# Optimization experiments

Hardware: AMD Instinct MI355X
Metric: run time of the kernel (lower is better)

The kernel has to match this reference:

```python
import jax, jax.numpy as jnp
import numpy as np

S, B, D = 2048, 2, 1024
NH, DH, DI = 16, 64, 4096


def setup_inputs() -> dict:
    key = jax.random.key(0)
    ks = jax.random.split(key, 12)
    init_qkv = 1.0 / np.sqrt(D)
    init_out = 1.0 / np.sqrt(NH * DH)
    stdm = 1.0 / np.sqrt(D)
    stdi = 1.0 / np.sqrt(DI)

    def u(k, shape, lo, hi):
        return jax.random.uniform(k, shape, jnp.float32, lo, hi)

    inp = {}
    inp["dec_inp"] = jax.random.normal(ks[0], (S, B, D), jnp.float32)
    # causal mask: True = masked (future key j > query i); shape [q, k, batch]
    causal = jnp.triu(jnp.ones((S, S), bool), k=1)
    inp["attn_mask"] = jnp.broadcast_to(causal[:, :, None], (S, S, B))
    inp["query_mean"] = u(ks[1], (NH * DH, D), -init_qkv, init_qkv)
    inp["key_mean"] = u(ks[2], (NH * DH, D), -init_qkv, init_qkv)
    inp["value_mean"] = u(ks[3], (NH * DH, D), -init_qkv, init_qkv)
    inp["query_std"] = u(ks[4], (NH * DH, D), 2 * np.log(init_qkv), np.log(init_qkv))
    inp["key_std"] = u(ks[5], (NH * DH, D), 2 * np.log(init_qkv), np.log(init_qkv))
    inp["value_std"] = u(ks[6], (NH * DH, D), 2 * np.log(init_qkv), np.log(init_qkv))
    inp["output_mean"] = u(ks[7], (D, NH * DH), -init_out, init_out)
    inp["output_std"] = u(ks[8], (D, NH * DH), 2 * np.log(init_out), np.log(init_out))
    inp["ln1_gamma"] = jnp.ones((D,), jnp.float32)
    inp["ln1_beta"] = jnp.zeros((D,), jnp.float32)
    inp["w1_mean"] = u(ks[9], (DI, D), -stdm, stdm)
    inp["w2_mean"] = u(ks[10], (D, DI), -stdi, stdi)
    inp["w1_std"] = u(ks[11], (DI, D), 2 * np.log(stdm), np.log(stdm))
    inp["w2_std"] = u(jax.random.fold_in(key, 99), (D, DI), 2 * np.log(stdi), np.log(stdi))
    inp["ln2_gamma"] = jnp.ones((D,), jnp.float32)
    inp["ln2_beta"] = jnp.zeros((D,), jnp.float32)
    return inp


def _layer_norm(x, g, b, eps=1e-5):
    mu = jnp.mean(x, -1, keepdims=True)
    var = jnp.mean((x - mu) ** 2, -1, keepdims=True)
    return g * (x - mu) * jax.lax.rsqrt(var + eps) + b


def _kl(theta_mean, theta_std):
    return jnp.mean(theta_mean ** 2 - 2.0 * theta_std + jnp.exp(2.0 * theta_std)) / 2.0


def reference(dec_inp, attn_mask, query_mean, key_mean, value_mean, query_std,
              key_std, value_std, output_mean, output_std, ln1_gamma, ln1_beta,
              w1_mean, w2_mean, w1_std, w2_std, ln2_gamma, ln2_beta):
    scale = 1.0 / (DH ** 0.5)
    # QKV projections (eval mode: no Bayesian weight sampling, diffs are 0)
    head_q = jnp.einsum('ibd,hd->ibh', dec_inp, query_mean).reshape(S, B, NH, DH)
    head_k = jnp.einsum('ibd,hd->ibh', dec_inp, key_mean).reshape(S, B, NH, DH)
    head_v = jnp.einsum('ibd,hd->ibh', dec_inp, value_mean).reshape(S, B, NH, DH)
    attn_score = jnp.einsum('ibnd,jbnd->ijbn', head_q, head_k) * scale
    attn_score = jnp.where(attn_mask[:, :, :, None], -jnp.inf, attn_score)
    attn_prob = jax.nn.softmax(attn_score, axis=1)  # softmax over key dim j
    attn_vec = jnp.einsum('ijbn,jbnd->ibnd', attn_prob, head_v).reshape(S, B, NH * DH)
    # NOTE: the original code (bug-faithfully) projects with value_mean, not output_mean
    attn_out = jnp.einsum('ibh,dh->ibd', attn_vec, value_mean)
    h = _layer_norm(dec_inp + attn_out, ln1_gamma, ln1_beta)
    attn_kl = _kl(
        jnp.concatenate([query_mean, key_mean, value_mean, output_mean.T], -1),
        jnp.concatenate([query_std, key_std, value_std, output_std.T], -1))
    # Bayesian positionwise FF (no activation in BayesPositionwiseFF)
    l1 = jnp.einsum('ibd,fd->ibf', h, w1_mean)
    l2 = jnp.einsum('ibf,df->ibd', l1, w2_mean)
    out = _layer_norm(h + l2, ln2_gamma, ln2_beta)
    ff_kl = _kl(jnp.concatenate([w1_mean, w2_mean.T], -1),
                jnp.concatenate([w1_std, w2_std.T], -1))
    return out, attn_kl + ff_kl
```

## Files before the change

kernel.cpp:

```cpp
#include <hip/hip_runtime.h>

#define S_LEN  2048
#define BATCH  2
#define DMODEL 1024
#define NHEADS 16
#define DHEAD  64
#define DFF    4096
#define MROWS  (S_LEN*BATCH)
#define QKVN   3072

typedef __attribute__((ext_vector_type(8))) short bf16x8;
typedef __attribute__((ext_vector_type(4))) float f32x4;
typedef __attribute__((ext_vector_type(4))) short s16x4;

#define NEG_BIG (-3.0e38f)
#define SCALE_LOG2 (0.125f * 1.4426950408889634f)

__device__ __forceinline__ short f2bf(float f){
  unsigned u = __float_as_uint(f);
  u += 0x7fffu + ((u >> 16) & 1u);
  return (short)(u >> 16);
}

__device__ __forceinline__ void gload16(const void* gptr, void* lptr){
  __builtin_amdgcn_global_load_lds(
      (const __attribute__((address_space(1))) unsigned int*)gptr,
      (__attribute__((address_space(3))) unsigned int*)lptr,
      16, 0, 0);
}

__global__ __launch_bounds__(256) void cast_kernel(const float* __restrict__ in,
                                                   short* __restrict__ out, int n){
  int i = (blockIdx.x * 256 + threadIdx.x) * 4;
  if (i >= n) return;
  f32x4 v = *(const f32x4*)(in + i);
  s16x4 o;
  o[0] = f2bf(v[0]); o[1] = f2bf(v[1]); o[2] = f2bf(v[2]); o[3] = f2bf(v[3]);
  *(s16x4*)(out + i) = o;
}

__global__ __launch_bounds__(512) void gemm_bt(const short* __restrict__ A,
                                               const short* __restrict__ Bt,
                                               float* __restrict__ Cf,
                                               short* __restrict__ Cb,
                                               int M, int N, int K){
  __shared__ short As[128][32];
  __shared__ short Bs[128][32];
  const int t = threadIdx.x;
  const int lane = t & 63, w = t >> 6;
  const int m0 = blockIdx.y * 128, n0 = blockIdx.x * 128;
  const int wm = (w & 3) * 32, wn = (w >> 2) * 64;
  const int lr = lane & 15, lg = lane >> 4;

  f32x4 acc[2][4] = {};

  const short* Ap = A  + (size_t)(m0 + (t >> 2)) * K + (t & 3) * 8;
  const short* Bp = Bt + (size_t)(n0 + (t >> 2)) * K + (t & 3) * 8;
  char* ldsA = (char*)(&As[0][0]) + w * 1024;
  char* ldsB = (char*)(&Bs[0][0]) + w * 1024;

  for (int k0 = 0; k0 < K; k0 += 32){
    gload16(Ap + k0, ldsA);
    gload16(Bp + k0, ldsB);
    __syncthreads();
    bf16x8 a0 = *(const bf16x8*)&As[wm      + lr][lg * 8];
    bf16x8 a1 = *(const bf16x8*)&As[wm + 16 + lr][lg * 8];
    bf16x8 b0 = *(const bf16x8*)&Bs[wn      + lr][lg * 8];
    bf16x8 b1 = *(const bf16x8*)&Bs[wn + 16 + lr][lg * 8];
    bf16x8 b2 = *(const bf16x8*)&Bs[wn + 32 + lr][lg * 8];
    bf16x8 b3 = *(const bf16x8*)&Bs[wn + 48 + lr][lg * 8];
    acc[0][0] = __builtin_amdgcn_mfma_f32_16x16x32_bf16(a0, b0, acc[0][0], 0, 0, 0);
    acc[0][1] = __builtin_amdgcn_mfma_f32_16x16x32_bf16(a0, b1, acc[0][1], 0, 0, 0);
    acc[0][2] = __builtin_amdgcn_mfma_f32_16x16x32_bf16(a0, b2, acc[0][2], 0, 0, 0);
    acc[0][3] = __builtin_amdgcn_mfma_f32_16x16x32_bf16(a0, b3, acc[0][3], 0, 0, 0);
    acc[1][0] = __builtin_amdgcn_mfma_f32_16x16x32_bf16(a1, b0, acc[1][0], 0, 0, 0);
    acc[1][1] = __builtin_amdgcn_mfma_f32_16x16x32_bf16(a1, b1, acc[1][1], 0, 0, 0);
    acc[1][2] = __builtin_amdgcn_mfma_f32_16x16x32_bf16(a1, b2, acc[1][2], 0, 0, 0);
    acc[1][3] = __builtin_amdgcn_mfma_f32_16x16x32_bf16(a1, b3, acc[1][3], 0, 0, 0);
    __syncthreads();
  }

  for (int mi = 0; mi < 2; mi++){
    for (int ni = 0; ni < 4; ni++){
      int row = m0 + wm + mi * 16 + lg * 4;
      int col = n0 + wn + ni * 16 + lr;
      for (int r = 0; r < 4; r++){
        float v = acc[mi][ni][r];
        if (Cf) Cf[(size_t)(row + r) * N + col] = v;
        if (Cb) Cb[(size_t)(row + r) * N + col] = f2bf(v);
      }
    }
  }
}

__global__ __launch_bounds__(256) void attn_kernel(const short* __restrict__ QKV,
                                                   short* __restrict__ AV){
  __shared__ short Ks[64][64];
  __shared__ short Vst[64][64];
  __shared__ short Ps[4][16][64];
  const int t = threadIdx.x, lane = t & 63, w = t >> 6;
  const int hb = blockIdx.y;
  const int b = hb >> 4, n = hb & 15;
  const int lr = lane & 15, lg = lane >> 4;

  for (int half = 0; half < 2; half++){
    const int qt = half ? (31 - (int)blockIdx.x) : (int)blockIdx.x;
    const int q0 = qt * 64 + w * 16;

    bf16x8 aq[2];
    {
      const short* qp = QKV + ((size_t)(q0 + lr) * BATCH + b) * QKVN + n * DHEAD + lg * 8;
      aq[0] = *(const bf16x8*)(qp);
      aq[1] = *(const bf16x8*)(qp + 32);
    }

    f32x4 acc[4] = {};
    float m_run[4], l_run[4];
    for (int r = 0; r < 4; r++){ m_run[r] = NEG_BIG; l_run[r] = 0.f; }

    const int njt = qt + 1;
    for (int jt = 0; jt < njt; jt++){
      const int j0 = jt * 64;
      __syncthreads();
      {
        int j = t >> 2, u0 = (t & 3) * 2;
        const short* kp = QKV + ((size_t)(j0 + j) * BATCH + b) * QKVN + DMODEL + n * DHEAD + u0 * 8;
        *(bf16x8*)&Ks[j][(u0 ^ (j & 7)) * 8]       = *(const bf16x8*)(kp);
        *(bf16x8*)&Ks[j][((u0 + 1) ^ (j & 7)) * 8] = *(const bf16x8*)(kp + 8);
        int jv = t & 63, dq = (t >> 6) * 16;
        const short* vp = QKV + ((size_t)(j0 + jv) * BATCH + b) * QKVN + 2 * DMODEL + n * DHEAD + dq;
        bf16x8 v0 = *(const bf16x8*)(vp);
        bf16x8 v1 = *(const bf16x8*)(vp + 8);
        int uj = jv >> 3, jl = jv & 7;
        for (int e = 0; e < 8; e++){
          int sc = (((uj ^ e) << 3) | jl);
          Vst[dq + e][sc]     = v0[e];
          Vst[dq + 8 + e][sc] = v1[e];
        }
      }
      __syncthreads();

      f32x4 s[4];
      __builtin_amdgcn_s_setprio(1);
      for (int nf = 0; nf < 4; nf++){
        f32x4 z = {};
        for (int kk = 0; kk < 2; kk++){
          int row = nf * 16 + lr;
          bf16x8 bk = *(const bf16x8*)&Ks[row][((kk * 4 + lg) ^ (lr & 7)) * 8];
          z = __builtin_amdgcn_mfma_f32_16x16x32_bf16(aq[kk], bk, z, 0, 0, 0);
        }
        s[nf] = z;
      }
      __builtin_amdgcn_s_setprio(0);

      for (int r = 0; r < 4; r++){
        int i_glob = q0 + lg * 4 + r;
        float mx = NEG_BIG;
        for (int nf = 0; nf < 4; nf++){
          int j_glob = j0 + nf * 16 + lr;
          float v = s[nf][r] * SCALE_LOG2;
          if (j_glob > i_glob) v = NEG_BIG;
          s[nf][r] = v;
          mx = fmaxf(mx, v);
        }
        for (int msk = 1; msk < 16; msk <<= 1) mx = fmaxf(mx, __shfl_xor(mx, msk, 64));
        float mn = fmaxf(m_run[r], mx);
        float corr = __builtin_exp2f(m_run[r] - mn);
        m_run[r] = mn;
        l_run[r] *= corr;
        for (int df = 0; df < 4; df++) acc[df][r] *= corr;
      }
      for (int r = 0; r < 4; r++){
        int prow = lg * 4 + r;
        float rs = 0.f;
        for (int nf = 0; nf < 4; nf++){
          float p = __builtin_exp2f(s[nf][r] - m_run[r]);
          rs += p;
          int u = (nf * 2) + (lr >> 3);
          Ps[w][prow][((u ^ (prow & 7)) << 3) | (lr & 7)] = f2bf(p);
        }
        for (int msk = 1; msk < 16; msk <<= 1) rs += __shfl_xor(rs, msk, 64);
        l_run[r] += rs;
      }
      __builtin_amdgcn_s_setprio(1);
      for (int kk = 0; kk < 2; kk++){
        bf16x8 pa = *(const bf16x8*)&Ps[w][lr][((kk * 4 + lg) ^ (lr & 7)) * 8];
        for (int df = 0; df < 4; df++){
          int row = df * 16 + lr;
          bf16x8 bv = *(const bf16x8*)&Vst[row][((kk * 4 + lg) ^ (lr & 7)) * 8];
          acc[df] = __builtin_amdgcn_mfma_f32_16x16x32_bf16(pa, bv, acc[df], 0, 0, 0);
        }
      }
      __builtin_amdgcn_s_setprio(0);
    }

    for (int df = 0; df < 4; df++){
      for (int r = 0; r < 4; r++){
        int i_glob = q0 + lg * 4 + r;
        AV[((size_t)i_glob * BATCH + b) * DMODEL + n * DHEAD + df * 16 + lr] =
            f2bf(acc[df][r] / l_run[r]);
      }
    }
    __syncthreads();
  }
}

__global__ __launch_bounds__(256) void ln_kernel(const float* __restrict__ xa,
                                                 const float* __restrict__ xb,
                                                 const float* __restrict__ gamma,
                                                 const float* __restrict__ beta,
                                                 float* __restrict__ outF,
                                                 short* __restrict__ outB){
  __shared__ float red[4];
  const int row = blockIdx.x, t = threadIdx.x;
  const size_t base = (size_t)row * DMODEL + t * 4;
  f32x4 a  = *(const f32x4*)(xa + base);
  f32x4 bb = *(const f32x4*)(xb + base);
  f32x4 x;
  for (int e = 0; e < 4; e++) x[e] = a[e] + bb[e];
  float sum = x[0] + x[1] + x[2] + x[3];
  for (int m = 1; m < 64; m <<= 1) sum += __shfl_xor(sum, m, 64);
  if ((t & 63) == 0) red[t >> 6] = sum;
  __syncthreads();
  float mu = (red[0] + red[1] + red[2] + red[3]) * (1.f / DMODEL);
  float sq = 0.f;
  for (int e = 0; e < 4; e++){ float d = x[e] - mu; sq += d * d; }
  for (int m = 1; m < 64; m <<= 1) sq += __shfl_xor(sq, m, 64);
  __syncthreads();
  if ((t & 63) == 0) red[t >> 6] = sq;
  __syncthreads();
  float var = (red[0] + red[1] + red[2] + red[3]) * (1.f / DMODEL);
  float rstd = rsqrtf(var + 1e-5f);
  f32x4 g  = *(const f32x4*)(gamma + t * 4);
  f32x4 be = *(const f32x4*)(beta + t * 4);
  for (int e = 0; e < 4; e++){
    float y = g[e] * (x[e] - mu) * rstd + be[e];
    if (outF) outF[base + e] = y;
    if (outB) outB[base + e] = f2bf(y);
  }
}

__global__ __launch_bounds__(256) void kl_kernel(const float* __restrict__ mean,
                                                 const float* __restrict__ stdv,
                                                 int n, double* acc){
  __shared__ double red[4];
  double local = 0.0;
  int stride = gridDim.x * 256;
  for (int i = blockIdx.x * 256 + threadIdx.x; i < n; i += stride){
    float m = mean[i], s = stdv[i];
    local += (double)(m * m) - 2.0 * (double)s + (double)expf(2.f * s);
  }
  for (int msk = 1; msk < 64; msk <<= 1) local += __shfl_xor(local, msk, 64);
  const int t = threadIdx.x;
  if ((t & 63) == 0) red[t >> 6] = local;
  __syncthreads();
  if (t == 0) atomicAdd(acc, red[0] + red[1] + red[2] + red[3]);
}

__global__ void kl_final(const double* acc, float* out){
  out[0] = (float)(acc[0] / 8388608.0 + acc[1] / 16777216.0);
}

extern "C" void kernel_launch(void* const* d_in, const int* in_sizes, int n_in,
                              void* d_out, int out_size, void* d_ws, size_t ws_size,
                              hipStream_t stream){
  (void)in_sizes; (void)n_in; (void)out_size; (void)ws_size;
  const float* dec = (const float*)d_in[0];
  const float* qm  = (const float*)d_in[2];
  const float* km  = (const float*)d_in[3];
  const float* vm  = (const float*)d_in[4];
  const float* qs  = (const float*)d_in[5];
  const float* ks  = (const float*)d_in[6];
  const float* vs  = (const float*)d_in[7];
  const float* om  = (const float*)d_in[8];
  const float* os_ = (const float*)d_in[9];
  const float* g1  = (const float*)d_in[10];
  const float* b1  = (const float*)d_in[11];
  const float* w1m = (const float*)d_in[12];
  const float* w2m = (const float*)d_in[13];
  const float* w1s = (const float*)d_in[14];
  const float* w2s = (const float*)d_in[15];
  const float* g2  = (const float*)d_in[16];
  const float* b2  = (const float*)d_in[17];
  float* out = (float*)d_out;

  char* ws = (char*)d_ws;
  size_t off = 0;
  auto alloc = [&](size_t bytes) -> char* {
    char* p = ws + off;
    off += (bytes + 255) & ~(size_t)255;
    return p;
  };
  short* Xb   = (short*)alloc((size_t)MROWS * DMODEL * 2);
  short* Wqkv = (short*)alloc((size_t)QKVN * DMODEL * 2);
  short* W1   = (short*)alloc((size_t)DFF * DMODEL * 2);
  short* W2   = (short*)alloc((size_t)DMODEL * DFF * 2);
  short* Wv   = Wqkv + (size_t)2 * DMODEL * DMODEL;
  short* QKVb = (short*)alloc((size_t)MROWS * QKVN * 2);
  short* AVb  = (short*)alloc((size_t)MROWS * DMODEL * 2);
  float* tmpF = (float*)alloc((size_t)MROWS * DMODEL * 4);
  float* hF   = (float*)alloc((size_t)MROWS * DMODEL * 4);
  double* acc = (double*)alloc(256);
  short* L1 = QKVb;

  hipMemsetAsync(acc, 0, 16, stream);

  cast_kernel<<<MROWS * DMODEL / 1024, 256, 0, stream>>>(dec, Xb, MROWS * DMODEL);
  cast_kernel<<<DMODEL * DMODEL / 1024, 256, 0, stream>>>(qm, Wqkv, DMODEL * DMODEL);
  cast_kernel<<<DMODEL * DMODEL / 1024, 256, 0, stream>>>(km, Wqkv + (size_t)DMODEL * DMODEL, DMODEL * DMODEL);
  cast_kernel<<<DMODEL * DMODEL / 1024, 256, 0, stream>>>(vm, Wqkv + (size_t)2 * DMODEL * DMODEL, DMODEL * DMODEL);
  cast_kernel<<<DFF * DMODEL / 1024, 256, 0, stream>>>(w1m, W1, DFF * DMODEL);
  cast_kernel<<<DMODEL * DFF / 1024, 256, 0, stream>>>(w2m, W2, DMODEL * DFF);

  gemm_bt<<<dim3(QKVN / 128, MROWS / 128), 512, 0, stream>>>(Xb, Wqkv, nullptr, QKVb, MROWS, QKVN, DMODEL);

  attn_kernel<<<dim3(16, BATCH * NHEADS), 256, 0, stream>>>(QKVb, AVb);

  gemm_bt<<<dim3(DMODEL / 128, MROWS / 128), 512, 0, stream>>>(AVb, Wv, tmpF, nullptr, MROWS, DMODEL, DMODEL);

  ln_kernel<<<MROWS, 256, 0, stream>>>(dec, tmpF, g1, b1, hF, Xb);

  gemm_bt<<<dim3(DFF / 128, MROWS / 128), 512, 0, stream>>>(Xb, W1, nullptr, L1, MROWS, DFF, DMODEL);
  gemm_bt<<<dim3(DMODEL / 128, MROWS / 128), 512, 0, stream>>>(L1, W2, tmpF, nullptr, MROWS, DMODEL, DFF);

  ln_kernel<<<MROWS, 256, 0, stream>>>(hF, tmpF, g2, b2, out, nullptr);

  kl_kernel<<<1024, 256, 0, stream>>>(qm, qs, DMODEL * DMODEL, acc);
  kl_kernel<<<1024, 256, 0, stream>>>(km, ks, DMODEL * DMODEL, acc);
  kl_kernel<<<1024, 256, 0, stream>>>(vm, vs, DMODEL * DMODEL, acc);
  kl_kernel<<<1024, 256, 0, stream>>>(om, os_, DMODEL * DMODEL, acc);
  kl_kernel<<<1024, 256, 0, stream>>>(w1m, w1s, DFF * DMODEL, acc + 1);
  kl_kernel<<<1024, 256, 0, stream>>>(w2m, w2s, DMODEL * DFF, acc + 1);
  kl_final<<<1, 1, 0, stream>>>(acc, out + (size_t)MROWS * DMODEL);
}
```

Before: 591.9 us.

## Template GEMM N-tile for narrow outputs and transpose attention score layout

The GEMM is templated on its N tile width. The two GEMMs with N=1024 now use a 64-wide tile, doubling their block count and filling more compute units. The attention kernel swaps the MFMA operands so each lane holds one query row. This lets the softmax max and sum reductions use two cross-lane shuffles instead of four per row. Causal masking is now applied only on the diagonal tile, and P is packed to bf16 by truncation instead of rounding, which slightly changes numerics.

Result: faster. 542.3 us (-8.4%).

```diff
diff --git a/kernel.cpp b/kernel.cpp
--- a/kernel.cpp
+++ b/kernel.cpp
@@ -39,49 +39,46 @@
   *(s16x4*)(out + i) = o;
 }
 
+template<int BN>
 __global__ __launch_bounds__(512) void gemm_bt(const short* __restrict__ A,
                                                const short* __restrict__ Bt,
                                                float* __restrict__ Cf,
                                                short* __restrict__ Cb,
                                                int M, int N, int K){
   __shared__ short As[128][32];
-  __shared__ short Bs[128][32];
+  __shared__ short Bs[BN][32];
+  constexpr int NB = BN / 32;
   const int t = threadIdx.x;
   const int lane = t & 63, w = t >> 6;
-  const int m0 = blockIdx.y * 128, n0 = blockIdx.x * 128;
-  const int wm = (w & 3) * 32, wn = (w >> 2) * 64;
+  const int m0 = blockIdx.y * 128, n0 = blockIdx.x * BN;
+  const int wm = (w & 3) * 32, wn = (w >> 2) * (BN / 2);
   const int lr = lane & 15, lg = lane >> 4;
 
-  f32x4 acc[2][4] = {};
+  f32x4 acc[2][NB] = {};
 
   const short* Ap = A  + (size_t)(m0 + (t >> 2)) * K + (t & 3) * 8;
-  const short* Bp = Bt + (size_t)(n0 + (t >> 2)) * K + (t & 3) * 8;
+  const short* Bp = Bt + (size_t)(n0 + ((t & (BN * 4 - 1)) >> 2)) * K + (t & 3) * 8;
   char* ldsA = (char*)(&As[0][0]) + w * 1024;
-  char* ldsB = (char*)(&Bs[0][0]) + w * 1024;
+  char* ldsB = (char*)(&Bs[0][0]) + (w & (BN / 32 * 2 - 1)) * 1024;
 
   for (int k0 = 0; k0 < K; k0 += 32){
     gload16(Ap + k0, ldsA);
-    gload16(Bp + k0, ldsB);
+    if (BN == 128 || t < 256) gload16(Bp + k0, ldsB);
     __syncthreads();
     bf16x8 a0 = *(const bf16x8*)&As[wm      + lr][lg * 8];
     bf16x8 a1 = *(const bf16x8*)&As[wm + 16 + lr][lg * 8];
-    bf16x8 b0 = *(const bf16x8*)&Bs[wn      + lr][lg * 8];
-    bf16x8 b1 = *(const bf16x8*)&Bs[wn + 16 + lr][lg * 8];
-    bf16x8 b2 = *(const bf16x8*)&Bs[wn + 32 + lr][lg * 8];
-    bf16x8 b3 = *(const bf16x8*)&Bs[wn + 48 + lr][lg * 8];
-    acc[0][0] = __builtin_amdgcn_mfma_f32_16x16x32_bf16(a0, b0, acc[0][0], 0, 0, 0);
-    acc[0][1] = __builtin_amdgcn_mfma_f32_16x16x32_bf16(a0, b1, acc[0][1], 0, 0, 0);
-    acc[0][2] = __builtin_amdgcn_mfma_f32_16x16x32_bf16(a0, b2, acc[0][2], 0, 0, 0);
-    acc[0][3] = __builtin_amdgcn_mfma_f32_16x16x32_bf16(a0, b3, acc[0][3], 0, 0, 0);
-    acc[1][0] = __builtin_amdgcn_mfma_f32_16x16x32_bf16(a1, b0, acc[1][0], 0, 0, 0);
-    acc[1][1] = __builtin_amdgcn_mfma_f32_16x16x32_bf16(a1, b1, acc[1][1], 0, 0, 0);
-    acc[1][2] = __builtin_amdgcn_mfma_f32_16x16x32_bf16(a1, b2, acc[1][2], 0, 0, 0);
-    acc[1][3] = __builtin_amdgcn_mfma_f32_16x16x32_bf16(a1, b3, acc[1][3], 0, 0, 0);
+    bf16x8 bfr[NB];
+    for (int ni = 0; ni < NB; ni++)
+      bfr[ni] = *(const bf16x8*)&Bs[wn + ni * 16 + lr][lg * 8];
+    for (int ni = 0; ni < NB; ni++){
+      acc[0][ni] = __builtin_amdgcn_mfma_f32_16x16x32_bf16(a0, bfr[ni], acc[0][ni], 0, 0, 0);
+      acc[1][ni] = __builtin_amdgcn_mfma_f32_16x16x32_bf16(a1, bfr[ni], acc[1][ni], 0, 0, 0);
+    }
     __syncthreads();
   }
 
   for (int mi = 0; mi < 2; mi++){
-    for (int ni = 0; ni < 4; ni++){
+    for (int ni = 0; ni < NB; ni++){
       int row = m0 + wm + mi * 16 + lg * 4;
       int col = n0 + wn + ni * 16 + lr;
       for (int r = 0; r < 4; r++){
@@ -97,7 +94,7 @@
                                                    short* __restrict__ AV){
   __shared__ short Ks[64][64];
   __shared__ short Vst[64][64];
-  __shared__ short Ps[4][16][64];
+  __shared__ short Pt[4][16][64];
   const int t = threadIdx.x, lane = t & 63, w = t >> 6;
   const int hb = blockIdx.y;
   const int b = hb >> 4, n = hb & 15;
@@ -105,21 +102,19 @@
 
   for (int half = 0; half < 2; half++){
     const int qt = half ? (31 - (int)blockIdx.x) : (int)blockIdx.x;
-    const int q0 = qt * 64 + w * 16;
+    const int q0w = qt * 64 + w * 16;
 
     bf16x8 aq[2];
     {
-      const short* qp = QKV + ((size_t)(q0 + lr) * BATCH + b) * QKVN + n * DHEAD + lg * 8;
+      const short* qp = QKV + ((size_t)(q0w + lr) * BATCH + b) * QKVN + n * DHEAD + lg * 8;
       aq[0] = *(const bf16x8*)(qp);
       aq[1] = *(const bf16x8*)(qp + 32);
     }
 
     f32x4 acc[4] = {};
-    float m_run[4], l_run[4];
-    for (int r = 0; r < 4; r++){ m_run[r] = NEG_BIG; l_run[r] = 0.f; }
-
-    const int njt = qt + 1;
-    for (int jt = 0; jt < njt; jt++){
+    float m_run = NEG_BIG, l_run = 0.f;
+
+    for (int jt = 0; jt <= qt; jt++){
       const int j0 = jt * 64;
       __syncthreads();
       {
@@ -145,60 +140,82 @@
       for (int nf = 0; nf < 4; nf++){
         f32x4 z = {};
         for (int kk = 0; kk < 2; kk++){
-          int row = nf * 16 + lr;
-          bf16x8 bk = *(const bf16x8*)&Ks[row][((kk * 4 + lg) ^ (lr & 7)) * 8];
-          z = __builtin_amdgcn_mfma_f32_16x16x32_bf16(aq[kk], bk, z, 0, 0, 0);
+          bf16x8 bk = *(const bf16x8*)&Ks[nf * 16 + lr][((kk * 4 + lg) ^ (lr & 7)) * 8];
+          z = __builtin_amdgcn_mfma_f32_16x16x32_bf16(bk, aq[kk], z, 0, 0, 0);
         }
         s[nf] = z;
       }
       __builtin_amdgcn_s_setprio(0);
 
-      for (int r = 0; r < 4; r++){
-        int i_glob = q0 + lg * 4 + r;
-        float mx = NEG_BIG;
-        for (int nf = 0; nf < 4; nf++){
-          int j_glob = j0 + nf * 16 + lr;
-          float v = s[nf][r] * SCALE_LOG2;
-          if (j_glob > i_glob) v = NEG_BIG;
-          s[nf][r] = v;
-          mx = fmaxf(mx, v);
+      for (int nf = 0; nf < 4; nf++)
+        for (int r = 0; r < 4; r++) s[nf][r] *= SCALE_LOG2;
+
+      if (jt == qt){
+        int qg = q0w + lr;
+        for (int nf = 0; nf < 4; nf++)
+          for (int r = 0; r < 4; r++)
+            if (j0 + nf * 16 + lg * 4 + r > qg) s[nf][r] = NEG_BIG;
+      }
+
+      float mx = NEG_BIG;
+      for (int nf = 0; nf < 4; nf++){
+        float a0 = fmaxf(s[nf][0], s[nf][1]);
+        float a1 = fmaxf(s[nf][2], s[nf][3]);
+        mx = fmaxf(mx, fmaxf(a0, a1));
+      }
+      mx = fmaxf(mx, __shfl_xor(mx, 16, 64));
+      mx = fmaxf(mx, __shfl_xor(mx, 32, 64));
+      float mn = fmaxf(m_run, mx);
+      float corr = __builtin_exp2f(m_run - mn);
+      m_run = mn;
+
+      float rs = 0.f;
+      for (int nf = 0; nf < 4; nf++)
+        for (int r = 0; r < 4; r++){
+          float p = __builtin_exp2f(s[nf][r] - mn);
+          s[nf][r] = p;
+          rs += p;
         }
-        for (int msk = 1; msk < 16; msk <<= 1) mx = fmaxf(mx, __shfl_xor(mx, msk, 64));
-        float mn = fmaxf(m_run[r], mx);
-        float corr = __builtin_exp2f(m_run[r] - mn);
-        m_run[r] = mn;
-        l_run[r] *= corr;
-        for (int df = 0; df < 4; df++) acc[df][r] *= corr;
-      }
-      for (int r = 0; r < 4; r++){
-        int prow = lg * 4 + r;
-        float rs = 0.f;
-        for (int nf = 0; nf < 4; nf++){
-          float p = __builtin_exp2f(s[nf][r] - m_run[r]);
-          rs += p;
-          int u = (nf * 2) + (lr >> 3);
-          Ps[w][prow][((u ^ (prow & 7)) << 3) | (lr & 7)] = f2bf(p);
-        }
-        for (int msk = 1; msk < 16; msk <<= 1) rs += __shfl_xor(rs, msk, 64);
-        l_run[r] += rs;
-      }
+      rs += __shfl_xor(rs, 16, 64);
+      rs += __shfl_xor(rs, 32, 64);
+      l_run = l_run * corr + rs;
+
+      char* prow = (char*)&Pt[w][lr][0];
+      for (int nf = 0; nf < 4; nf++){
+        unsigned u0 = __float_as_uint(s[nf][0]);
+        unsigned u1 = __float_as_uint(s[nf][1]);
+        unsigned u2 = __float_as_uint(s[nf][2]);
+        unsigned u3 = __float_as_uint(s[nf][3]);
+        uint2 val;
+        val.x = (u0 >> 16) | (u1 & 0xffff0000u);
+        val.y = (u2 >> 16) | (u3 & 0xffff0000u);
+        int off = ((((nf * 2) + (lg >> 1)) ^ (lr & 7)) << 4) + ((lg & 1) << 3);
+        *(uint2*)(prow + off) = val;
+      }
+
+      float cb[4];
+      for (int r = 0; r < 4; r++) cb[r] = __shfl(corr, lg * 4 + r, 64);
+      for (int df = 0; df < 4; df++)
+        for (int r = 0; r < 4; r++) acc[df][r] *= cb[r];
+
       __builtin_amdgcn_s_setprio(1);
       for (int kk = 0; kk < 2; kk++){
-        bf16x8 pa = *(const bf16x8*)&Ps[w][lr][((kk * 4 + lg) ^ (lr & 7)) * 8];
+        bf16x8 pa = *(const bf16x8*)(prow + ((((kk * 4) + lg) ^ (lr & 7)) << 4));
         for (int df = 0; df < 4; df++){
-          int row = df * 16 + lr;
-          bf16x8 bv = *(const bf16x8*)&Vst[row][((kk * 4 + lg) ^ (lr & 7)) * 8];
+          bf16x8 bv = *(const bf16x8*)&Vst[df * 16 + lr][((kk * 4 + lg) ^ (lr & 7)) * 8];
           acc[df] = __builtin_amdgcn_mfma_f32_16x16x32_bf16(pa, bv, acc[df], 0, 0, 0);
         }
       }
       __builtin_amdgcn_s_setprio(0);
     }
 
+    float lb[4];
+    for (int r = 0; r < 4; r++) lb[r] = __shfl(l_run, lg * 4 + r, 64);
     for (int df = 0; df < 4; df++){
       for (int r = 0; r < 4; r++){
-        int i_glob = q0 + lg * 4 + r;
+        int i_glob = q0w + lg * 4 + r;
         AV[((size_t)i_glob * BATCH + b) * DMODEL + n * DHEAD + df * 16 + lr] =
-            f2bf(acc[df][r] / l_run[r]);
+            f2bf(acc[df][r] / lb[r]);
       }
     }
     __syncthreads();
@@ -312,16 +329,16 @@
   cast_kernel<<<DFF * DMODEL / 1024, 256, 0, stream>>>(w1m, W1, DFF * DMODEL);
   cast_kernel<<<DMODEL * DFF / 1024, 256, 0, stream>>>(w2m, W2, DMODEL * DFF);
 
-  gemm_bt<<<dim3(QKVN / 128, MROWS / 128), 512, 0, stream>>>(Xb, Wqkv, nullptr, QKVb, MROWS, QKVN, DMODEL);
+  gemm_bt<128><<<dim3(QKVN / 128, MROWS / 128), 512, 0, stream>>>(Xb, Wqkv, nullptr, QKVb, MROWS, QKVN, DMODEL);
 
   attn_kernel<<<dim3(16, BATCH * NHEADS), 256, 0, stream>>>(QKVb, AVb);
 
-  gemm_bt<<<dim3(DMODEL / 128, MROWS / 128), 512, 0, stream>>>(AVb, Wv, tmpF, nullptr, MROWS, DMODEL, DMODEL);
+  gemm_bt<64><<<dim3(DMODEL / 64, MROWS / 128), 512, 0, stream>>>(AVb, Wv, tmpF, nullptr, MROWS, DMODEL, DMODEL);
 
   ln_kernel<<<MROWS, 256, 0, stream>>>(dec, tmpF, g1, b1, hF, Xb);
 
-  gemm_bt<<<dim3(DFF / 128, MROWS / 128), 512, 0, stream>>>(Xb, W1, nullptr, L1, MROWS, DFF, DMODEL);
-  gemm_bt<<<dim3(DMODEL / 128, MROWS / 128), 512, 0, stream>>>(L1, W2, tmpF, nullptr, MROWS, DMODEL, DFF);
+  gemm_bt<128><<<dim3(DFF / 128, MROWS / 128), 512, 0, stream>>>(Xb, W1, nullptr, L1, MROWS, DFF, DMODEL);
+  gemm_bt<64><<<dim3(DMODEL / 64, MROWS / 128), 512, 0, stream>>>(L1, W2, tmpF, nullptr, MROWS, DMODEL, DFF);
 
   ln_kernel<<<MROWS, 256, 0, stream>>>(hF, tmpF, g2, b2, out, nullptr);
 
```
